# Optimization experiments

Measured on AMD Instinct MI355X. Metric: run time of the kernel, lower is better.

The kernel has to match this reference:

```python
import jax, jax.numpy as jnp
import numpy as np

DIM = 1024
HIDDEN = 4096
NUM_EXPERTS = 8
TOP_K = 2


def setup_inputs() -> dict:
    key = jax.random.key(0)
    ks = jax.random.split(key, 7)
    x = jax.random.normal(ks[0], (4, 2048, DIM), dtype=jnp.float32)
    # router Linear(dim, num_experts)
    Wr = jax.random.normal(ks[1], (DIM, NUM_EXPERTS), dtype=jnp.float32) / np.sqrt(DIM)
    br = jnp.zeros((NUM_EXPERTS,), dtype=jnp.float32)
    # stacked expert weights: Linear(dim, hidden) -> GELU -> Linear(hidden, dim)
    W1 = jax.random.normal(ks[2], (NUM_EXPERTS, DIM, HIDDEN), dtype=jnp.float32) / np.sqrt(DIM)
    b1 = jnp.zeros((NUM_EXPERTS, HIDDEN), dtype=jnp.float32)
    W2 = jax.random.normal(ks[3], (NUM_EXPERTS, HIDDEN, DIM), dtype=jnp.float32) / np.sqrt(HIDDEN)
    b2 = jnp.zeros((NUM_EXPERTS, DIM), dtype=jnp.float32)
    return {"x": x, "Wr": Wr, "br": br, "W1": W1, "b1": b1, "W2": W2, "b2": b2}


def reference(x, Wr, br, W1, b1, W2, b2):
    # router: g_x = W_e x ; p = softmax(g_x)
    logits = jnp.einsum('bsd,de->bse', x, Wr) + br            # [B,S,E]
    probs = jax.nn.softmax(logits, axis=-1)
    topk_probs, topk_idx = jax.lax.top_k(probs, TOP_K)        # [B,S,K]
    # dense compute-all-experts (faithful to torch.stack over experts)
    h = jnp.einsum('bsd,edh->bseh', x, W1) + b1               # [B,S,E,H]
    h = jax.nn.gelu(h, approximate=False)                      # torch nn.GELU default = exact erf
    expert_out = jnp.einsum('bseh,ehd->bsed', h, W2) + b2     # [B,S,E,D]
    # gather top-k expert outputs and mix
    selected = jnp.take_along_axis(expert_out, topk_idx[..., None], axis=2)  # [B,S,K,D]
    mixed = jnp.sum(topk_probs[..., None] * selected, axis=2)                # [B,S,D]
    return mixed, logits, probs, topk_idx, topk_probs
```

## Files before the change

### kernel.cpp

```cpp
#include <hip/hip_runtime.h>
#include <hip/hip_bf16.h>
#include <math.h>
#include <stdint.h>

#define DIMD 1024
#define HIDDEN 4096
#define NE 8
#define TOPK_ 2
#define T_TOKENS 8192
#define NROWS (T_TOKENS * TOPK_)
#define BK 64
#define BM1 128
#define BN1 256
#define BM2 128
#define BN2 128
#define MAXTILES (NROWS / 128 + NE)
#define TGS 8
#define NRB (T_TOKENS / 8)
#define NW2T 2048

typedef __bf16 bf16_t;
typedef __bf16 bf16x8 __attribute__((ext_vector_type(8)));
typedef float f32x4 __attribute__((ext_vector_type(4)));

__device__ __forceinline__ void glds16(const void* g, void* l) {
    __builtin_amdgcn_global_load_lds(
        (const __attribute__((address_space(1))) unsigned int*)g,
        (__attribute__((address_space(3))) unsigned int*)l, 16, 0, 0);
}

__device__ __forceinline__ bf16x8 ldfrag(const char* lds_, int row, int kelem) {
    int byte = row * 128 + ((kelem * 2) ^ ((row & 7) << 4));
    return *reinterpret_cast<const bf16x8*>(lds_ + byte);
}

__device__ __forceinline__ int xcd_contig(int bid, int nwg) {
    int xcd = bid & 7;
    int lid = bid >> 3;
    int q = nwg >> 3, r = nwg & 7;
    int base = (xcd < r) ? xcd * (q + 1) : r * (q + 1) + (xcd - r) * q;
    return base + lid;
}

__device__ __forceinline__ void transpose_tile(
    const float* __restrict__ in, bf16_t* __restrict__ out,
    int K, int N, int kt, int nt, char* ldsraw)
{
    bf16_t (*tile)[136] = reinterpret_cast<bf16_t(*)[136]>(ldsraw);
    int k0 = kt * 128, n0 = nt * 128;
    const float* ip = in + (size_t)k0 * N + n0;
    bf16_t* op = out + (size_t)n0 * K + k0;
    int t = threadIdx.x;
    int r = t >> 2;
    int q = t & 3;
    const float* rp = ip + (size_t)r * N + q * 32;
    bf16_t* trow = &tile[r][q * 32];
#pragma unroll
    for (int i = 0; i < 4; ++i) {
        float4 a = *reinterpret_cast<const float4*>(rp + i * 8);
        float4 b = *reinterpret_cast<const float4*>(rp + i * 8 + 4);
        bf16x8 o;
        o[0] = (bf16_t)a.x; o[1] = (bf16_t)a.y; o[2] = (bf16_t)a.z; o[3] = (bf16_t)a.w;
        o[4] = (bf16_t)b.x; o[5] = (bf16_t)b.y; o[6] = (bf16_t)b.z; o[7] = (bf16_t)b.w;
        *reinterpret_cast<bf16x8*>(trow + i * 8) = o;
    }
    __syncthreads();
    int nn = t >> 2;
    bf16_t* wp = op + (size_t)nn * K + q * 32;
#pragma unroll
    for (int i = 0; i < 4; ++i) {
        bf16x8 o;
#pragma unroll
        for (int j = 0; j < 8; ++j) o[j] = tile[q * 32 + i * 8 + j][nn];
        *reinterpret_cast<bf16x8*>(wp + i * 8) = o;
    }
}

__global__ __launch_bounds__(512) void prologue_kernel(
    const float* __restrict__ x, const float* __restrict__ Wr, const float* __restrict__ br,
    const float* __restrict__ W1,
    float* __restrict__ logits, float* __restrict__ probs,
    float* __restrict__ tidx, float* __restrict__ tprob,
    int* __restrict__ cnt, bf16_t* __restrict__ Xb,
    bf16_t* __restrict__ W1T)
{
    __shared__ __align__(16) char ldsraw[34816];
    int bid0 = blockIdx.x;
    if (bid0 < NRB) {
        int wave = threadIdx.x >> 6;
        int lane = threadIdx.x & 63;
        int t = bid0 * 8 + wave;
        const float* xr = x + (size_t)t * DIMD;
        double acc[NE];
#pragma unroll
        for (int e = 0; e < NE; ++e) acc[e] = 0.0;
        for (int i = 0; i < DIMD / 64; ++i) {
            int d = i * 64 + lane;
            double xv = (double)xr[d];
            float4 w0 = *reinterpret_cast<const float4*>(Wr + d * NE);
            float4 w1 = *reinterpret_cast<const float4*>(Wr + d * NE + 4);
            acc[0] += xv * (double)w0.x; acc[1] += xv * (double)w0.y;
            acc[2] += xv * (double)w0.z; acc[3] += xv * (double)w0.w;
            acc[4] += xv * (double)w1.x; acc[5] += xv * (double)w1.y;
            acc[6] += xv * (double)w1.z; acc[7] += xv * (double)w1.w;
        }
#pragma unroll
        for (int s = 32; s >= 1; s >>= 1) {
#pragma unroll
            for (int e = 0; e < NE; ++e) acc[e] += __shfl_xor(acc[e], s, 64);
        }
        if (lane == 0) {
            double lg[NE], mx = -1e300;
#pragma unroll
            for (int e = 0; e < NE; ++e) { lg[e] = acc[e] + (double)br[e]; mx = fmax(mx, lg[e]); }
            int i0 = 0; double l0 = -1e300;
#pragma unroll
            for (int e = 0; e < NE; ++e) { if (lg[e] > l0) { l0 = lg[e]; i0 = e; } }
            int i1 = -1; double l1 = -1e300;
#pragma unroll
            for (int e = 0; e < NE; ++e) { if (e == i0) continue; if (lg[e] > l1) { l1 = lg[e]; i1 = e; } }
            float pe[NE], s = 0.f;
#pragma unroll
            for (int e = 0; e < NE; ++e) { pe[e] = __expf((float)(lg[e] - mx)); s += pe[e]; }
            float inv = 1.f / s;
#pragma unroll
            for (int e = 0; e < NE; ++e) {
                pe[e] *= inv;
                logits[t * NE + e] = (float)lg[e];
                probs[t * NE + e] = pe[e];
            }
            tidx[t * 2 + 0] = (float)i0; tidx[t * 2 + 1] = (float)i1;
            tprob[t * 2 + 0] = pe[i0];   tprob[t * 2 + 1] = pe[i1];
            atomicAdd(&cnt[i0], 1); atomicAdd(&cnt[i1], 1);
        }
#pragma unroll
        for (int j = 0; j < 2; ++j) {
            int i = (j * 64 + lane) * 8;
            float4 a = *reinterpret_cast<const float4*>(xr + i);
            float4 b = *reinterpret_cast<const float4*>(xr + i + 4);
            bf16x8 o;
            o[0] = (bf16_t)a.x; o[1] = (bf16_t)a.y; o[2] = (bf16_t)a.z; o[3] = (bf16_t)a.w;
            o[4] = (bf16_t)b.x; o[5] = (bf16_t)b.y; o[6] = (bf16_t)b.z; o[7] = (bf16_t)b.w;
            *reinterpret_cast<bf16x8*>(Xb + (size_t)t * DIMD + i) = o;
        }
        return;
    }
    int bid = bid0 - NRB;
    int e = bid >> 8;
    int rem = bid & 255;
    int kt = rem >> 5, nt = rem & 31;
    transpose_tile(W1 + (size_t)e * DIMD * HIDDEN, W1T + (size_t)e * HIDDEN * DIMD,
                   DIMD, HIDDEN, kt, nt, ldsraw);
}

__global__ __launch_bounds__(256) void prefix_kernel(
    const int* __restrict__ cnt, int* __restrict__ offsets,
    int* __restrict__ tileE, int* __restrict__ tileRow, int* __restrict__ numTiles)
{
    __shared__ int soff[NE + 1], scnt[NE];
    int t = threadIdx.x;
    if (t == 0) {
        int off = 0;
        for (int e = 0; e < NE; ++e) { scnt[e] = cnt[e]; soff[e] = off; off += scnt[e]; }
        soff[NE] = off;
        int nt = 0;
        for (int e = 0; e < NE; ++e) nt += (scnt[e] + 127) / 128;
        *numTiles = nt;
    }
    __syncthreads();
    if (t <= NE) offsets[t] = soff[t];
    if (t < MAXTILES) {
        int acc = 0;
#pragma unroll
        for (int e = 0; e < NE; ++e) {
            int ntE = (scnt[e] + 127) / 128;
            if (t < acc + ntE) { tileE[t] = e; tileRow[t] = soff[e] + (t - acc) * 128; return; }
            acc += ntE;
        }
    }
}

__global__ __launch_bounds__(256) void scatter_kernel(
    const float* __restrict__ tidx, const float* __restrict__ tprob,
    const int* __restrict__ offsets, int* __restrict__ gcursor,
    int* __restrict__ rowToken, int* __restrict__ tokRow)
{
    __shared__ int lcnt[NE], lbase[NE];
    int t = blockIdx.x * 256 + threadIdx.x;
    if (threadIdx.x < NE) lcnt[threadIdx.x] = 0;
    __syncthreads();
    int e0 = (int)tidx[t * 2 + 0], e1 = (int)tidx[t * 2 + 1];
    int r0l = atomicAdd(&lcnt[e0], 1);
    int r1l = atomicAdd(&lcnt[e1], 1);
    __syncthreads();
    if (threadIdx.x < NE) lbase[threadIdx.x] = atomicAdd(&gcursor[threadIdx.x], lcnt[threadIdx.x]);
    __syncthreads();
    int r0 = offsets[e0] + lbase[e0] + r0l;
    int r1 = offsets[e1] + lbase[e1] + r1l;
    rowToken[r0] = t; rowToken[r1] = t;
    tokRow[t * 2 + 0] = r0; tokRow[t * 2 + 1] = r1;
}

__global__ __launch_bounds__(512) void ffn1_kernel(
    const bf16_t* __restrict__ Xb, const bf16_t* __restrict__ W1T, const float* __restrict__ b1,
    const float* __restrict__ W2, bf16_t* __restrict__ W2T,
    const int* __restrict__ tileE, const int* __restrict__ tileRow, const int* __restrict__ numTiles,
    const int* __restrict__ offsets, const int* __restrict__ rowToken,
    bf16_t* __restrict__ h)
{
    __shared__ __align__(16) char lds[49152];
    int bid0 = blockIdx.x;
    if (bid0 < NW2T) {
        int e = bid0 >> 8;
        int rem = bid0 & 255;
        int kt = rem >> 3, nt = rem & 7;
        transpose_tile(W2 + (size_t)e * HIDDEN * DIMD, W2T + (size_t)e * DIMD * HIDDEN,
                       HIDDEN, DIMD, kt, nt, lds);
        return;
    }
    const int NB = HIDDEN / BN1;
    int logical = xcd_contig(bid0 - NW2T, gridDim.x - NW2T);
    int tg  = logical / (NB * TGS);
    int rem = logical % (NB * TGS);
    int nb  = rem / TGS;
    int ti  = rem % TGS;
    int tile = tg * TGS + ti;
    if (tile >= *numTiles) return;
    int e = tileE[tile];
    int row0 = tileRow[tile];
    int rend = offsets[e + 1];
    int n0 = nb * BN1;

    int tid = threadIdx.x;
    int lane = tid & 63;
    int wid = tid >> 6;
    int wr = (wid >> 2) * 64;
    int wc = (wid & 3) * 64;
    int rr = lane & 15;
    int k4 = (lane >> 4) * 8;

    int srow = tid >> 3;
    int xc = (((tid & 7) ^ (srow & 7)) << 4);
    const char *pa0, *pa1, *pb0, *pb1, *pb2, *pb3;
    {
        int g0 = row0 + srow;      if (g0 > NROWS - 1) g0 = NROWS - 1;
        int g1 = row0 + 64 + srow; if (g1 > NROWS - 1) g1 = NROWS - 1;
        pa0 = (const char*)(Xb + (size_t)rowToken[g0] * DIMD) + xc;
        pa1 = (const char*)(Xb + (size_t)rowToken[g1] * DIMD) + xc;
        pb0 = (const char*)(W1T + ((size_t)e * HIDDEN + n0 + srow) * DIMD) + xc;
        pb1 = (const char*)(W1T + ((size_t)e * HIDDEN + n0 + 64 + srow) * DIMD) + xc;
        pb2 = (const char*)(W1T + ((size_t)e * HIDDEN + n0 + 128 + srow) * DIMD) + xc;
        pb3 = (const char*)(W1T + ((size_t)e * HIDDEN + n0 + 192 + srow) * DIMD) + xc;
    }

    f32x4 acc[4][4];
#pragma unroll
    for (int i = 0; i < 4; ++i)
#pragma unroll
        for (int j = 0; j < 4; ++j) acc[i][j] = f32x4{0.f, 0.f, 0.f, 0.f};

    for (int t_ = 0; t_ < DIMD / BK; ++t_) {
        int kb = t_ * 128;
        glds16(pa0 + kb, lds + wid * 1024);
        glds16(pa1 + kb, lds + 8192 + wid * 1024);
        glds16(pb0 + kb, lds + 16384 + wid * 1024);
        glds16(pb1 + kb, lds + 24576 + wid * 1024);
        glds16(pb2 + kb, lds + 32768 + wid * 1024);
        glds16(pb3 + kb, lds + 40960 + wid * 1024);
        __syncthreads();
#pragma unroll
        for (int ks = 0; ks < 2; ++ks) {
            int kk = ks * 32 + k4;
            bf16x8 b_[4], a_[4];
#pragma unroll
            for (int n = 0; n < 4; ++n) b_[n] = ldfrag(lds + 16384, wc + n * 16 + rr, kk);
#pragma unroll
            for (int m = 0; m < 4; ++m) a_[m] = ldfrag(lds, wr + m * 16 + rr, kk);
#pragma unroll
            for (int m = 0; m < 4; ++m)
#pragma unroll
                for (int n = 0; n < 4; ++n)
                    acc[m][n] = __builtin_amdgcn_mfma_f32_16x16x32_bf16(a_[m], b_[n], acc[m][n], 0, 0, 0);
        }
        __syncthreads();
    }

    int crow = (lane >> 4) * 4;
    int ccol = lane & 15;
#pragma unroll
    for (int m = 0; m < 4; ++m) {
#pragma unroll
        for (int n = 0; n < 4; ++n) {
            int col = wc + n * 16 + ccol;
            float bias = b1[e * HIDDEN + n0 + col];
#pragma unroll
            for (int r = 0; r < 4; ++r) {
                int row = row0 + wr + m * 16 + crow + r;
                if (row < rend) {
                    float v = acc[m][n][r] + bias;
                    float g = 0.5f * v * (1.0f + erff(v * 0.70710678118654752f));
                    h[(size_t)row * HIDDEN + n0 + col] = (bf16_t)g;
                }
            }
        }
    }
}

__global__ __launch_bounds__(256) void ffn2_kernel(
    const bf16_t* __restrict__ h, const bf16_t* __restrict__ W2T, const float* __restrict__ b2,
    const int* __restrict__ tileE, const int* __restrict__ tileRow, const int* __restrict__ numTiles,
    const int* __restrict__ offsets, float* __restrict__ part)
{
    const int NB = DIMD / BN2;
    int logical = xcd_contig(blockIdx.x, gridDim.x);
    int tile = logical / NB;
    int nb = logical % NB;
    if (tile >= *numTiles) return;
    int e = tileE[tile];
    int row0 = tileRow[tile];
    int rend = offsets[e + 1];
    int n0 = nb * BN2;

    __shared__ __align__(16) char lds[32768];

    int tid = threadIdx.x;
    int lane = tid & 63;
    int wid = tid >> 6;
    int wr = (wid >> 1) * 64;
    int wc = (wid & 1) * 64;
    int rr = lane & 15;
    int k4 = (lane >> 4) * 8;

    int srow = tid >> 3;
    int xc = (((tid & 7) ^ (srow & 7)) << 4);
    const char *pa0, *pa1, *pa2, *pa3, *pb0, *pb1, *pb2, *pb3;
    {
        int g0 = row0 + srow;      if (g0 > NROWS - 1) g0 = NROWS - 1;
        int g1 = row0 + 32 + srow; if (g1 > NROWS - 1) g1 = NROWS - 1;
        int g2 = row0 + 64 + srow; if (g2 > NROWS - 1) g2 = NROWS - 1;
        int g3 = row0 + 96 + srow; if (g3 > NROWS - 1) g3 = NROWS - 1;
        pa0 = (const char*)(h + (size_t)g0 * HIDDEN) + xc;
        pa1 = (const char*)(h + (size_t)g1 * HIDDEN) + xc;
        pa2 = (const char*)(h + (size_t)g2 * HIDDEN) + xc;
        pa3 = (const char*)(h + (size_t)g3 * HIDDEN) + xc;
        pb0 = (const char*)(W2T + ((size_t)e * DIMD + n0 + srow) * HIDDEN) + xc;
        pb1 = (const char*)(W2T + ((size_t)e * DIMD + n0 + 32 + srow) * HIDDEN) + xc;
        pb2 = (const char*)(W2T + ((size_t)e * DIMD + n0 + 64 + srow) * HIDDEN) + xc;
        pb3 = (const char*)(W2T + ((size_t)e * DIMD + n0 + 96 + srow) * HIDDEN) + xc;
    }

    f32x4 acc[4][4];
#pragma unroll
    for (int i = 0; i < 4; ++i)
#pragma unroll
        for (int j = 0; j < 4; ++j) acc[i][j] = f32x4{0.f, 0.f, 0.f, 0.f};

    for (int t_ = 0; t_ < HIDDEN / BK; ++t_) {
        int kb = t_ * 128;
        char* dA = lds + wid * 1024;
        char* dB = lds + 16384 + wid * 1024;
        glds16(pa0 + kb, dA);          glds16(pb0 + kb, dB);
        glds16(pa1 + kb, dA + 4096);   glds16(pb1 + kb, dB + 4096);
        glds16(pa2 + kb, dA + 8192);   glds16(pb2 + kb, dB + 8192);
        glds16(pa3 + kb, dA + 12288);  glds16(pb3 + kb, dB + 12288);
        __syncthreads();
#pragma unroll
        for (int ks = 0; ks < 2; ++ks) {
            int kk = ks * 32 + k4;
            bf16x8 a_[4], b_[4];
#pragma unroll
            for (int m = 0; m < 4; ++m) a_[m] = ldfrag(lds, wr + m * 16 + rr, kk);
#pragma unroll
            for (int n = 0; n < 4; ++n) b_[n] = ldfrag(lds + 16384, wc + n * 16 + rr, kk);
#pragma unroll
            for (int m = 0; m < 4; ++m)
#pragma unroll
                for (int n = 0; n < 4; ++n)
                    acc[m][n] = __builtin_amdgcn_mfma_f32_16x16x32_bf16(a_[m], b_[n], acc[m][n], 0, 0, 0);
        }
        __syncthreads();
    }

    int crow = (lane >> 4) * 4;
    int ccol = lane & 15;
#pragma unroll
    for (int m = 0; m < 4; ++m) {
#pragma unroll
        for (int n = 0; n < 4; ++n) {
            int col = wc + n * 16 + ccol;
            int dcol = n0 + col;
            float bias = b2[e * DIMD + dcol];
#pragma unroll
            for (int r = 0; r < 4; ++r) {
                int row = row0 + wr + m * 16 + crow + r;
                if (row < rend) {
                    part[(size_t)row * DIMD + dcol] = acc[m][n][r] + bias;
                }
            }
        }
    }
}

__global__ __launch_bounds__(256) void reduce_kernel(
    const float* __restrict__ part, const float* __restrict__ tprob,
    const int* __restrict__ tokRow, float* __restrict__ mixed)
{
    int idx = blockIdx.x * 256 + threadIdx.x;
    int tok = idx >> 8;
    int q = (idx & 255) * 4;
    int r0 = tokRow[tok * 2 + 0], r1 = tokRow[tok * 2 + 1];
    float p0 = tprob[tok * 2 + 0], p1 = tprob[tok * 2 + 1];
    float4 a = *reinterpret_cast<const float4*>(part + (size_t)r0 * DIMD + q);
    float4 b = *reinterpret_cast<const float4*>(part + (size_t)r1 * DIMD + q);
    float4 o;
    o.x = p0 * a.x + p1 * b.x;
    o.y = p0 * a.y + p1 * b.y;
    o.z = p0 * a.z + p1 * b.z;
    o.w = p0 * a.w + p1 * b.w;
    *reinterpret_cast<float4*>(mixed + (size_t)tok * DIMD + q) = o;
}

extern "C" void kernel_launch(void* const* d_in, const int* in_sizes, int n_in,
                              void* d_out, int out_size, void* d_ws, size_t ws_size,
                              hipStream_t stream)
{
    const float* x  = (const float*)d_in[0];
    const float* Wr = (const float*)d_in[1];
    const float* br = (const float*)d_in[2];
    const float* W1 = (const float*)d_in[3];
    const float* b1 = (const float*)d_in[4];
    const float* W2 = (const float*)d_in[5];
    const float* b2 = (const float*)d_in[6];

    float* out = (float*)d_out;
    float* mixed  = out;
    float* logits = out + (size_t)T_TOKENS * DIMD;
    float* probs  = logits + T_TOKENS * NE;
    float* tidx   = probs + T_TOKENS * NE;
    float* tprob  = tidx + T_TOKENS * TOPK_;

    char* p = (char*)d_ws;
    auto alloc = [&](size_t bytes) { char* r = p; p += (bytes + 255) & ~255ull; return r; };
    int*    small    = (int*)alloc(2 * NE * 4);
    int*    cnt      = small;
    int*    gcursor  = small + NE;
    int*    offsets  = (int*)alloc((NE + 1) * 4);
    int*    numTiles = (int*)alloc(4);
    int*    tileE    = (int*)alloc(MAXTILES * 4);
    int*    tileRow  = (int*)alloc(MAXTILES * 4);
    int*    rowToken = (int*)alloc(NROWS * 4);
    int*    tokRow   = (int*)alloc(NROWS * 4);
    bf16_t* W1T      = (bf16_t*)alloc((size_t)NE * HIDDEN * DIMD * 2);
    bf16_t* W2T      = (bf16_t*)alloc((size_t)NE * DIMD * HIDDEN * 2);
    bf16_t* Xb       = (bf16_t*)alloc((size_t)T_TOKENS * DIMD * 2);
    bf16_t* hbuf     = (bf16_t*)alloc((size_t)NROWS * HIDDEN * 2);
    float*  part     = (float*)alloc((size_t)NROWS * DIMD * 4);

    hipMemsetAsync(small, 0, 2 * NE * 4, stream);

    prologue_kernel<<<NRB + 2048, 512, 0, stream>>>(
        x, Wr, br, W1, logits, probs, tidx, tprob, cnt, Xb, W1T);
    prefix_kernel<<<1, 256, 0, stream>>>(cnt, offsets, tileE, tileRow, numTiles);
    scatter_kernel<<<T_TOKENS / 256, 256, 0, stream>>>(tidx, tprob, offsets, gcursor, rowToken, tokRow);

    ffn1_kernel<<<NW2T + MAXTILES * (HIDDEN / BN1), 512, 0, stream>>>(
        Xb, W1T, b1, W2, W2T, tileE, tileRow, numTiles, offsets, rowToken, hbuf);
    ffn2_kernel<<<MAXTILES * (DIMD / BN2), 256, 0, stream>>>(
        hbuf, W2T, b2, tileE, tileRow, numTiles, offsets, part);
    reduce_kernel<<<T_TOKENS * DIMD / 4 / 256, 256, 0, stream>>>(part, tprob, tokRow, mixed);
}
```

Before: 730.2 us.

## Store transposed expert weights as contiguous 128x128 tiles; move W2 transpose to prologue

```diff
diff --git a/kernel.cpp b/kernel.cpp
--- a/kernel.cpp
+++ b/kernel.cpp
@@ -17,7 +17,6 @@
 #define MAXTILES (NROWS / 128 + NE)
 #define TGS 8
 #define NRB (T_TOKENS / 8)
-#define NW2T 2048
 
 typedef __bf16 bf16_t;
 typedef __bf16 bf16x8 __attribute__((ext_vector_type(8)));
@@ -47,9 +46,9 @@
     int K, int N, int kt, int nt, char* ldsraw)
 {
     bf16_t (*tile)[136] = reinterpret_cast<bf16_t(*)[136]>(ldsraw);
+    int KT = K >> 7;
     int k0 = kt * 128, n0 = nt * 128;
     const float* ip = in + (size_t)k0 * N + n0;
-    bf16_t* op = out + (size_t)n0 * K + k0;
     int t = threadIdx.x;
     int r = t >> 2;
     int q = t & 3;
@@ -66,7 +65,7 @@
     }
     __syncthreads();
     int nn = t >> 2;
-    bf16_t* wp = op + (size_t)nn * K + q * 32;
+    bf16_t* wp = out + (((size_t)(nt * KT + kt)) << 14) + nn * 128 + q * 32;
 #pragma unroll
     for (int i = 0; i < 4; ++i) {
         bf16x8 o;
@@ -78,11 +77,11 @@
 
 __global__ __launch_bounds__(512) void prologue_kernel(
     const float* __restrict__ x, const float* __restrict__ Wr, const float* __restrict__ br,
-    const float* __restrict__ W1,
+    const float* __restrict__ W1, const float* __restrict__ W2,
     float* __restrict__ logits, float* __restrict__ probs,
     float* __restrict__ tidx, float* __restrict__ tprob,
     int* __restrict__ cnt, bf16_t* __restrict__ Xb,
-    bf16_t* __restrict__ W1T)
+    bf16_t* __restrict__ W1T, bf16_t* __restrict__ W2T)
 {
     __shared__ __align__(16) char ldsraw[34816];
     int bid0 = blockIdx.x;
@@ -146,11 +145,20 @@
         return;
     }
     int bid = bid0 - NRB;
-    int e = bid >> 8;
-    int rem = bid & 255;
-    int kt = rem >> 5, nt = rem & 31;
-    transpose_tile(W1 + (size_t)e * DIMD * HIDDEN, W1T + (size_t)e * HIDDEN * DIMD,
-                   DIMD, HIDDEN, kt, nt, ldsraw);
+    if (bid < 2048) {
+        int e = bid >> 8;
+        int rem = bid & 255;
+        int nt = rem >> 3, kt = rem & 7;
+        transpose_tile(W1 + (size_t)e * DIMD * HIDDEN, W1T + (size_t)e * HIDDEN * DIMD,
+                       DIMD, HIDDEN, kt, nt, ldsraw);
+    } else {
+        bid -= 2048;
+        int e = bid >> 8;
+        int rem = bid & 255;
+        int nt = rem >> 5, kt = rem & 31;
+        transpose_tile(W2 + (size_t)e * HIDDEN * DIMD, W2T + (size_t)e * DIMD * HIDDEN,
+                       HIDDEN, DIMD, kt, nt, ldsraw);
+    }
 }
 
 __global__ __launch_bounds__(256) void prefix_kernel(
@@ -203,23 +211,12 @@
 
 __global__ __launch_bounds__(512) void ffn1_kernel(
     const bf16_t* __restrict__ Xb, const bf16_t* __restrict__ W1T, const float* __restrict__ b1,
-    const float* __restrict__ W2, bf16_t* __restrict__ W2T,
     const int* __restrict__ tileE, const int* __restrict__ tileRow, const int* __restrict__ numTiles,
     const int* __restrict__ offsets, const int* __restrict__ rowToken,
     bf16_t* __restrict__ h)
 {
-    __shared__ __align__(16) char lds[49152];
-    int bid0 = blockIdx.x;
-    if (bid0 < NW2T) {
-        int e = bid0 >> 8;
-        int rem = bid0 & 255;
-        int kt = rem >> 3, nt = rem & 7;
-        transpose_tile(W2 + (size_t)e * HIDDEN * DIMD, W2T + (size_t)e * DIMD * HIDDEN,
-                       HIDDEN, DIMD, kt, nt, lds);
-        return;
-    }
     const int NB = HIDDEN / BN1;
-    int logical = xcd_contig(bid0 - NW2T, gridDim.x - NW2T);
+    int logical = xcd_contig(blockIdx.x, gridDim.x);
     int tg  = logical / (NB * TGS);
     int rem = logical % (NB * TGS);
     int nb  = rem / TGS;
@@ -231,6 +228,8 @@
     int rend = offsets[e + 1];
     int n0 = nb * BN1;
 
+    __shared__ __align__(16) char lds[49152];
+
     int tid = threadIdx.x;
     int lane = tid & 63;
     int wid = tid >> 6;
@@ -247,10 +246,14 @@
         int g1 = row0 + 64 + srow; if (g1 > NROWS - 1) g1 = NROWS - 1;
         pa0 = (const char*)(Xb + (size_t)rowToken[g0] * DIMD) + xc;
         pa1 = (const char*)(Xb + (size_t)rowToken[g1] * DIMD) + xc;
-        pb0 = (const char*)(W1T + ((size_t)e * HIDDEN + n0 + srow) * DIMD) + xc;
-        pb1 = (const char*)(W1T + ((size_t)e * HIDDEN + n0 + 64 + srow) * DIMD) + xc;
-        pb2 = (const char*)(W1T + ((size_t)e * HIDDEN + n0 + 128 + srow) * DIMD) + xc;
-        pb3 = (const char*)(W1T + ((size_t)e * HIDDEN + n0 + 192 + srow) * DIMD) + xc;
+        const char* wb = (const char*)W1T + (size_t)e * HIDDEN * DIMD * 2;
+#pragma unroll
+        for (int i = 0; i < 1; ++i) {}
+        int o0 = 0 * 64 + srow, o1 = 1 * 64 + srow, o2 = 2 * 64 + srow, o3 = 3 * 64 + srow;
+        pb0 = wb + (size_t)(nb * 2 + (o0 >> 7)) * 262144 + (size_t)(o0 & 127) * 256 + xc;
+        pb1 = wb + (size_t)(nb * 2 + (o1 >> 7)) * 262144 + (size_t)(o1 & 127) * 256 + xc;
+        pb2 = wb + (size_t)(nb * 2 + (o2 >> 7)) * 262144 + (size_t)(o2 & 127) * 256 + xc;
+        pb3 = wb + (size_t)(nb * 2 + (o3 >> 7)) * 262144 + (size_t)(o3 & 127) * 256 + xc;
     }
 
     f32x4 acc[4][4];
@@ -260,13 +263,14 @@
         for (int j = 0; j < 4; ++j) acc[i][j] = f32x4{0.f, 0.f, 0.f, 0.f};
 
     for (int t_ = 0; t_ < DIMD / BK; ++t_) {
-        int kb = t_ * 128;
-        glds16(pa0 + kb, lds + wid * 1024);
-        glds16(pa1 + kb, lds + 8192 + wid * 1024);
-        glds16(pb0 + kb, lds + 16384 + wid * 1024);
-        glds16(pb1 + kb, lds + 24576 + wid * 1024);
-        glds16(pb2 + kb, lds + 32768 + wid * 1024);
-        glds16(pb3 + kb, lds + 40960 + wid * 1024);
+        int kbA = t_ * 128;
+        int kbB = (t_ >> 1) * 32768 + (t_ & 1) * 128;
+        glds16(pa0 + kbA, lds + wid * 1024);
+        glds16(pa1 + kbA, lds + 8192 + wid * 1024);
+        glds16(pb0 + kbB, lds + 16384 + wid * 1024);
+        glds16(pb1 + kbB, lds + 24576 + wid * 1024);
+        glds16(pb2 + kbB, lds + 32768 + wid * 1024);
+        glds16(pb3 + kbB, lds + 40960 + wid * 1024);
         __syncthreads();
 #pragma unroll
         for (int ks = 0; ks < 2; ++ks) {
@@ -343,10 +347,11 @@
         pa1 = (const char*)(h + (size_t)g1 * HIDDEN) + xc;
         pa2 = (const char*)(h + (size_t)g2 * HIDDEN) + xc;
         pa3 = (const char*)(h + (size_t)g3 * HIDDEN) + xc;
-        pb0 = (const char*)(W2T + ((size_t)e * DIMD + n0 + srow) * HIDDEN) + xc;
-        pb1 = (const char*)(W2T + ((size_t)e * DIMD + n0 + 32 + srow) * HIDDEN) + xc;
-        pb2 = (const char*)(W2T + ((size_t)e * DIMD + n0 + 64 + srow) * HIDDEN) + xc;
-        pb3 = (const char*)(W2T + ((size_t)e * DIMD + n0 + 96 + srow) * HIDDEN) + xc;
+        const char* wb = (const char*)W2T + (size_t)e * DIMD * HIDDEN * 2 + (size_t)nb * 1048576;
+        pb0 = wb + (size_t)(0 * 32 + srow) * 256 + xc;
+        pb1 = wb + (size_t)(1 * 32 + srow) * 256 + xc;
+        pb2 = wb + (size_t)(2 * 32 + srow) * 256 + xc;
+        pb3 = wb + (size_t)(3 * 32 + srow) * 256 + xc;
     }
 
     f32x4 acc[4][4];
@@ -356,13 +361,14 @@
         for (int j = 0; j < 4; ++j) acc[i][j] = f32x4{0.f, 0.f, 0.f, 0.f};
 
     for (int t_ = 0; t_ < HIDDEN / BK; ++t_) {
-        int kb = t_ * 128;
+        int kbA = t_ * 128;
+        int kbB = (t_ >> 1) * 32768 + (t_ & 1) * 128;
         char* dA = lds + wid * 1024;
         char* dB = lds + 16384 + wid * 1024;
-        glds16(pa0 + kb, dA);          glds16(pb0 + kb, dB);
-        glds16(pa1 + kb, dA + 4096);   glds16(pb1 + kb, dB + 4096);
-        glds16(pa2 + kb, dA + 8192);   glds16(pb2 + kb, dB + 8192);
-        glds16(pa3 + kb, dA + 12288);  glds16(pb3 + kb, dB + 12288);
+        glds16(pa0 + kbA, dA);          glds16(pb0 + kbB, dB);
+        glds16(pa1 + kbA, dA + 4096);   glds16(pb1 + kbB, dB + 4096);
+        glds16(pa2 + kbA, dA + 8192);   glds16(pb2 + kbB, dB + 8192);
+        glds16(pa3 + kbA, dA + 12288);  glds16(pb3 + kbB, dB + 12288);
         __syncthreads();
 #pragma unroll
         for (int ks = 0; ks < 2; ++ks) {
@@ -458,13 +464,13 @@
 
     hipMemsetAsync(small, 0, 2 * NE * 4, stream);
 
-    prologue_kernel<<<NRB + 2048, 512, 0, stream>>>(
-        x, Wr, br, W1, logits, probs, tidx, tprob, cnt, Xb, W1T);
+    prologue_kernel<<<NRB + 4096, 512, 0, stream>>>(
+        x, Wr, br, W1, W2, logits, probs, tidx, tprob, cnt, Xb, W1T, W2T);
     prefix_kernel<<<1, 256, 0, stream>>>(cnt, offsets, tileE, tileRow, numTiles);
     scatter_kernel<<<T_TOKENS / 256, 256, 0, stream>>>(tidx, tprob, offsets, gcursor, rowToken, tokRow);
 
-    ffn1_kernel<<<NW2T + MAXTILES * (HIDDEN / BN1), 512, 0, stream>>>(
-        Xb, W1T, b1, W2, W2T, tileE, tileRow, numTiles, offsets, rowToken, hbuf);
+    ffn1_kernel<<<MAXTILES * (HIDDEN / BN1), 512, 0, stream>>>(
+        Xb, W1T, b1, tileE, tileRow, numTiles, offsets, rowToken, hbuf);
     ffn2_kernel<<<MAXTILES * (DIMD / BN2), 256, 0, stream>>>(
         hbuf, W2T, b2, tileE, tileRow, numTiles, offsets, part);
     reduce_kernel<<<T_TOKENS * DIMD / 4 / 256, 256, 0, stream>>>(part, tprob, tokRow, mixed);
```

New measurement: 794.9 us. 1.09x slower.
